# Performance work log

Measured on AMD Instinct MI355X. Metric: run time of the kernel, lower is better.

## Reference

```python
import jax, jax.numpy as jnp
import numpy as np


def _segment_mean(x, idx, num_segments):
    # mean-aggregate rows of x into num_segments buckets (PyG SAGEConv default aggr)
    s = jax.ops.segment_sum(x, idx, num_segments=num_segments)
    c = jax.ops.segment_sum(jnp.ones((idx.shape[0],), x.dtype), idx, num_segments=num_segments)
    return s / jnp.maximum(c, 1.0)[:, None]


def setup_inputs() -> dict:
    key = jax.random.key(0)
    ks = jax.random.split(key, 12)
    N_LIG, N_PROT, D, H, E = 100000, 50000, 64, 128, 2000000
    sc = 0.05
    return {
        "x_lig": jax.random.normal(ks[0], (N_LIG, D), jnp.float32),
        "x_prot": jax.random.normal(ks[1], (N_PROT, D), jnp.float32),
        "W_l_lp": jax.random.normal(ks[2], (D, H), jnp.float32) * sc,
        "b_lp": jnp.zeros((H,), jnp.float32),
        "W_r_lp": jax.random.normal(ks[3], (D, H), jnp.float32) * sc,
        "W_l_pl": jax.random.normal(ks[4], (D, H), jnp.float32) * sc,
        "b_pl": jnp.zeros((H,), jnp.float32),
        "W_r_pl": jax.random.normal(ks[5], (D, H), jnp.float32) * sc,
        "W_lin": jax.random.normal(ks[6], (H, 1), jnp.float32) * sc,
        "b_lin": jnp.zeros((1,), jnp.float32),
        "src_lp": jax.random.randint(ks[7], (E,), 0, N_LIG, jnp.int32),
        "dst_lp": jax.random.randint(ks[8], (E,), 0, N_PROT, jnp.int32),
        "src_pl": jax.random.randint(ks[9], (E,), 0, N_PROT, jnp.int32),
        "dst_pl": jax.random.randint(ks[10], (E,), 0, N_LIG, jnp.int32),
    }


def reference(x_lig, x_prot, W_l_lp, b_lp, W_r_lp, W_l_pl, b_pl, W_r_pl,
              W_lin, b_lin, src_lp, dst_lp, src_pl, dst_pl):
    n_lig = x_lig.shape[0]
    n_prot = x_prot.shape[0]
    # SAGEConv ('ligand','interacts','protein'): gather ligand feats along edges, mean into proteins
    agg_prot = _segment_mean(x_lig[src_lp], dst_lp, n_prot)          # [N_prot, D]
    h_prot = jax.nn.relu(agg_prot @ W_l_lp + b_lp + x_prot @ W_r_lp)  # [N_prot, H] (dead downstream, as in original)
    # SAGEConv ('protein','interacts','ligand')
    agg_lig = _segment_mean(x_prot[src_pl], dst_pl, n_lig)           # [N_lig, D]
    h_lig = jax.nn.relu(agg_lig @ W_l_pl + b_pl + x_lig @ W_r_pl)    # [N_lig, H]
    ligand_out = h_lig.mean(axis=0)                                  # [H]
    del h_prot  # original computes it but never uses it (only 'ligand' feeds the head)
    return ligand_out @ W_lin + b_lin                                # [1]
```

## Files before the change

kernel.cpp:

```cpp
#include <hip/hip_runtime.h>

#define D 64
#define H 128
#define BN 128
#define CAP 3456
#define NBB 256
#define CE 7816

typedef short bf16x8 __attribute__((ext_vector_type(8)));
typedef float f32x4  __attribute__((ext_vector_type(4)));

__device__ __forceinline__ ushort f2bf(float f) {
    unsigned u = __float_as_uint(f);
    unsigned r = (u + 0x7FFFu + ((u >> 16) & 1u)) >> 16;
    return (ushort)r;
}

__device__ __forceinline__ bf16x8 pack8(float4 a, float4 b) {
    ushort o[8];
    o[0]=f2bf(a.x); o[1]=f2bf(a.y); o[2]=f2bf(a.z); o[3]=f2bf(a.w);
    o[4]=f2bf(b.x); o[5]=f2bf(b.y); o[6]=f2bf(b.z); o[7]=f2bf(b.w);
    bf16x8 r;
    __builtin_memcpy(&r, o, 16);
    return r;
}

__global__ __launch_bounds__(256)
void stage1_kernel(const float* __restrict__ xp, ushort* __restrict__ xpb, int totalp,
                   const float* __restrict__ Wl, const float* __restrict__ Wr,
                   ushort* __restrict__ wprep,
                   const int* __restrict__ dst, int* __restrict__ cnt,
                   int E, int K, int ce, int PB) {
    __shared__ int scnt[800];
    int bid = blockIdx.x;
    int t = threadIdx.x;
    if (bid < PB) {
        int i = (bid * 256 + t) * 8;
        if (i < totalp) {
            float4 a = *(const float4*)(xp + i);
            float4 b = *(const float4*)(xp + i + 4);
            bf16x8 v = pack8(a, b);
            *(bf16x8*)(xpb + i) = v;
        }
    } else if (bid < PB + 8) {
        int e = (bid - PB) * 256 + t;
        if (e < 2048) {
            int lane = e & 63;
            int ks = (e >> 6) & 3;
            int ht = e >> 8;
            int h = ht * 16 + (lane & 15);
            int k0 = ks * 32 + (lane >> 4) * 8;
            ushort o[8];
            #pragma unroll
            for (int j = 0; j < 8; ++j) {
                int k = k0 + j;
                float v = (k < D) ? Wl[k * H + h] : Wr[(k - D) * H + h];
                o[j] = f2bf(v);
            }
            *(bf16x8*)(wprep + (size_t)e * 8) = *(bf16x8*)o;
        }
    } else {
        int blk = bid - PB - 8;
        for (int b = t; b < 800; b += 256) scnt[b] = 0;
        __syncthreads();
        int e0 = blk * ce;
        int e1 = min(E, e0 + ce);
        for (int i = e0 + t * 4; i < e1; i += 1024) {
            int4 d4 = *(const int4*)(dst + i);
            atomicAdd(&scnt[d4.x >> 7], 1);
            atomicAdd(&scnt[d4.y >> 7], 1);
            atomicAdd(&scnt[d4.z >> 7], 1);
            atomicAdd(&scnt[d4.w >> 7], 1);
        }
        __syncthreads();
        int* row = cnt + (size_t)blk * K;
        for (int b = t; b < K; b += 256) row[b] = scnt[b];
    }
}

__global__ __launch_bounds__(NBB)
void part_scan_kernel(const int* __restrict__ cnt, int* __restrict__ off,
                      int* __restrict__ tot, int K) {
    __shared__ int s[NBB];
    int b = blockIdx.x;
    int t = threadIdx.x;
    int v = cnt[(size_t)t * K + b];
    s[t] = v;
    __syncthreads();
    for (int o = 1; o < NBB; o <<= 1) {
        int x = (t >= o) ? s[t - o] : 0;
        __syncthreads();
        s[t] += x;
        __syncthreads();
    }
    off[(size_t)t * K + b] = s[t] - v;
    if (t == NBB - 1) tot[b] = s[t];
}

__global__ __launch_bounds__(512)
void part_scatter_kernel(const int* __restrict__ src, const int* __restrict__ dst,
                         const int* __restrict__ off, int* __restrict__ gb,
                         int E, int K, int ce) {
    __shared__ int shist[800];
    __shared__ int sbase[800];
    __shared__ int gdelta[800];
    __shared__ int lcur[800];
    __shared__ int sscan[512];
    __shared__ int ebuf[CE];
    __shared__ unsigned short bkt[CE];

    int blk = blockIdx.x, t = threadIdx.x;
    int e0 = blk * ce;
    int e1 = min(E, e0 + ce);
    int myn = e1 - e0;

    for (int b = t; b < 800; b += 512) shist[b] = 0;
    __syncthreads();
    for (int i = e0 + t * 4; i < e1; i += 2048) {
        int4 d4 = *(const int4*)(dst + i);
        atomicAdd(&shist[d4.x >> 7], 1);
        atomicAdd(&shist[d4.y >> 7], 1);
        atomicAdd(&shist[d4.z >> 7], 1);
        atomicAdd(&shist[d4.w >> 7], 1);
    }
    __syncthreads();
    int c0 = 0, c1 = 0;
    if (t < 400) { c0 = shist[2 * t]; c1 = shist[2 * t + 1]; }
    int cs = c0 + c1;
    sscan[t] = (t < 400) ? cs : 0;
    __syncthreads();
    for (int o = 1; o < 512; o <<= 1) {
        int x = (t >= o) ? sscan[t - o] : 0;
        __syncthreads();
        sscan[t] += x;
        __syncthreads();
    }
    if (t < 400) {
        int ex = sscan[t] - cs;
        sbase[2 * t] = ex;
        sbase[2 * t + 1] = ex + c0;
    }
    __syncthreads();
    const int* orow = off + (size_t)blk * K;
    for (int b = t; b < K; b += 512) {
        int sb = sbase[b];
        gdelta[b] = orow[b] - sb;
        lcur[b] = sb;
    }
    __syncthreads();
    for (int i = e0 + t * 4; i < e1; i += 2048) {
        int4 d4 = *(const int4*)(dst + i);
        int4 s4 = *(const int4*)(src + i);
        int b, p;
        b = d4.x >> 7; p = atomicAdd(&lcur[b], 1);
        ebuf[p] = (s4.x & 0xFFFF) | ((d4.x & 127) << 16); bkt[p] = (unsigned short)b;
        b = d4.y >> 7; p = atomicAdd(&lcur[b], 1);
        ebuf[p] = (s4.y & 0xFFFF) | ((d4.y & 127) << 16); bkt[p] = (unsigned short)b;
        b = d4.z >> 7; p = atomicAdd(&lcur[b], 1);
        ebuf[p] = (s4.z & 0xFFFF) | ((d4.z & 127) << 16); bkt[p] = (unsigned short)b;
        b = d4.w >> 7; p = atomicAdd(&lcur[b], 1);
        ebuf[p] = (s4.w & 0xFFFF) | ((d4.w & 127) << 16); bkt[p] = (unsigned short)b;
    }
    __syncthreads();
    for (int p = t; p < myn; p += 512) {
        int b = bkt[p];
        int loc = gdelta[b] + p;
        if (loc < CAP) gb[(size_t)b * CAP + loc] = ebuf[p];
    }
}

__global__ __launch_bounds__(512, 4)
void fused_kernel(const ushort* __restrict__ xpb, const float* __restrict__ x_lig,
                  const int* __restrict__ gtot, const int* __restrict__ gb,
                  const ushort* __restrict__ wprep, const float* __restrict__ bvec,
                  float* __restrict__ pgrid, int N) {
    __shared__ int sdeg[BN];
    __shared__ int sstart[BN];
    __shared__ int scur[BN];
    __shared__ int ssc[BN];
    __shared__ int scsr[CAP];
    __shared__ unsigned sxrow[8][16][34];
    __shared__ float sred[8][H];

    int b = blockIdx.x, t = threadIdx.x;
    int cnt = min(gtot[b], CAP);
    const int* mygb = gb + (size_t)b * CAP;

    if (t < BN) sdeg[t] = 0;
    __syncthreads();
    for (int i = t; i < cnt; i += 512)
        atomicAdd(&sdeg[mygb[i] >> 16], 1);
    __syncthreads();
    if (t < BN) ssc[t] = sdeg[t];
    __syncthreads();
    for (int off = 1; off < BN; off <<= 1) {
        int v = 0;
        if (t < BN && t >= off) v = ssc[t - off];
        __syncthreads();
        if (t < BN) ssc[t] += v;
        __syncthreads();
    }
    if (t < BN) {
        int ex = ssc[t] - sdeg[t];
        sstart[t] = ex;
        scur[t] = ex;
    }
    __syncthreads();
    for (int i = t; i < cnt; i += 512) {
        int e = mygb[i];
        int p = atomicAdd(&scur[e >> 16], 1);
        scsr[p] = e & 0xFFFF;
    }
    __syncthreads();

    int wv = t >> 6, lane = t & 63;
    int sub = lane >> 3, part = lane & 7;

    for (int i = 0; i < 16; ++i) {
        int ln = wv * 16 + i;
        int s0 = sstart[ln], dg = sdeg[ln];
        float a[8] = {0.f,0.f,0.f,0.f,0.f,0.f,0.f,0.f};
        int j = sub;
        for (; j + 8 < dg; j += 16) {
            uint4 v0 = *(const uint4*)(xpb + (size_t)scsr[s0 + j] * D + part * 8);
            uint4 v1 = *(const uint4*)(xpb + (size_t)scsr[s0 + j + 8] * D + part * 8);
            a[0] += __uint_as_float(v0.x << 16); a[1] += __uint_as_float(v0.x & 0xFFFF0000u);
            a[2] += __uint_as_float(v0.y << 16); a[3] += __uint_as_float(v0.y & 0xFFFF0000u);
            a[4] += __uint_as_float(v0.z << 16); a[5] += __uint_as_float(v0.z & 0xFFFF0000u);
            a[6] += __uint_as_float(v0.w << 16); a[7] += __uint_as_float(v0.w & 0xFFFF0000u);
            a[0] += __uint_as_float(v1.x << 16); a[1] += __uint_as_float(v1.x & 0xFFFF0000u);
            a[2] += __uint_as_float(v1.y << 16); a[3] += __uint_as_float(v1.y & 0xFFFF0000u);
            a[4] += __uint_as_float(v1.z << 16); a[5] += __uint_as_float(v1.z & 0xFFFF0000u);
            a[6] += __uint_as_float(v1.w << 16); a[7] += __uint_as_float(v1.w & 0xFFFF0000u);
        }
        if (j < dg) {
            uint4 v0 = *(const uint4*)(xpb + (size_t)scsr[s0 + j] * D + part * 8);
            a[0] += __uint_as_float(v0.x << 16); a[1] += __uint_as_float(v0.x & 0xFFFF0000u);
            a[2] += __uint_as_float(v0.y << 16); a[3] += __uint_as_float(v0.y & 0xFFFF0000u);
            a[4] += __uint_as_float(v0.z << 16); a[5] += __uint_as_float(v0.z & 0xFFFF0000u);
            a[6] += __uint_as_float(v0.w << 16); a[7] += __uint_as_float(v0.w & 0xFFFF0000u);
        }
        #pragma unroll
        for (int k = 0; k < 8; ++k) {
            a[k] += __shfl_xor(a[k], 8);
            a[k] += __shfl_xor(a[k], 16);
            a[k] += __shfl_xor(a[k], 32);
        }
        if (sub == 0) {
            float inv = 1.0f / fmaxf((float)dg, 1.0f);
            unsigned p0 = (unsigned)f2bf(a[0]*inv) | ((unsigned)f2bf(a[1]*inv) << 16);
            unsigned p1 = (unsigned)f2bf(a[2]*inv) | ((unsigned)f2bf(a[3]*inv) << 16);
            unsigned p2 = (unsigned)f2bf(a[4]*inv) | ((unsigned)f2bf(a[5]*inv) << 16);
            unsigned p3 = (unsigned)f2bf(a[6]*inv) | ((unsigned)f2bf(a[7]*inv) << 16);
            uint2* w2 = (uint2*)&sxrow[wv][i][part * 4];
            w2[0] = make_uint2(p0, p1);
            w2[1] = make_uint2(p2, p3);
        }
    }

    int r = lane & 15, kg = lane >> 4;

    unsigned ua0[4], ua1[4];
    const unsigned* rp = &sxrow[wv][r][0];
    #pragma unroll
    for (int j2 = 0; j2 < 4; ++j2) {
        ua0[j2] = rp[kg * 4 + j2];
        ua1[j2] = rp[16 + kg * 4 + j2];
    }
    bf16x8 A0, A1;
    __builtin_memcpy(&A0, ua0, 16);
    __builtin_memcpy(&A1, ua1, 16);

    int grow = b * BN + wv * 16 + r;
    bf16x8 A2, A3;
    if (grow < N) {
        const float* xr = x_lig + (size_t)grow * D;
        float4 va = *(const float4*)(xr + kg * 8);
        float4 vb = *(const float4*)(xr + kg * 8 + 4);
        A2 = pack8(va, vb);
        float4 vc = *(const float4*)(xr + 32 + kg * 8);
        float4 vd = *(const float4*)(xr + 32 + kg * 8 + 4);
        A3 = pack8(vc, vd);
    } else {
        A2 = bf16x8{0,0,0,0,0,0,0,0};
        A3 = A2;
    }

    float hsum[8];
    bool full = (b * BN + wv * 16 + 16 <= N);
    const bf16x8* wp = (const bf16x8*)wprep;
    #pragma unroll 2
    for (int ht = 0; ht < 8; ++ht) {
        f32x4 acc = {0.f, 0.f, 0.f, 0.f};
        acc = __builtin_amdgcn_mfma_f32_16x16x32_bf16(A0, wp[(ht*4+0)*64 + lane], acc, 0, 0, 0);
        acc = __builtin_amdgcn_mfma_f32_16x16x32_bf16(A1, wp[(ht*4+1)*64 + lane], acc, 0, 0, 0);
        acc = __builtin_amdgcn_mfma_f32_16x16x32_bf16(A2, wp[(ht*4+2)*64 + lane], acc, 0, 0, 0);
        acc = __builtin_amdgcn_mfma_f32_16x16x32_bf16(A3, wp[(ht*4+3)*64 + lane], acc, 0, 0, 0);
        float bb = bvec[ht * 16 + r];
        float s = 0.f;
        if (full) {
            #pragma unroll
            for (int i = 0; i < 4; ++i) s += fmaxf(acc[i] + bb, 0.f);
        } else {
            #pragma unroll
            for (int i = 0; i < 4; ++i) {
                int row = b * BN + wv * 16 + kg * 4 + i;
                if (row < N) s += fmaxf(acc[i] + bb, 0.f);
            }
        }
        hsum[ht] = s;
    }

    #pragma unroll
    for (int ht = 0; ht < 8; ++ht) {
        float v = hsum[ht];
        v += __shfl_xor(v, 16);
        v += __shfl_xor(v, 32);
        if (lane < 16) sred[wv][ht * 16 + lane] = v;
    }
    __syncthreads();
    if (t < H) {
        float s = 0.f;
        #pragma unroll
        for (int w = 0; w < 8; ++w) s += sred[w][t];
        pgrid[(size_t)b * H + t] = s;
    }
}

__global__ __launch_bounds__(128)
void reduce1_kernel(const float* __restrict__ pgrid, int nb, float* __restrict__ pgrid2) {
    int t = threadIdx.x;
    float s = 0.f;
    for (int r = blockIdx.x; r < nb; r += 64) s += pgrid[(size_t)r * H + t];
    pgrid2[(size_t)blockIdx.x * H + t] = s;
}

__global__ __launch_bounds__(128)
void head_kernel(const float* __restrict__ pgrid2,
                 const float* __restrict__ W_lin, const float* __restrict__ b_lin,
                 float* __restrict__ out, float invN) {
    __shared__ float sh[H];
    int t = threadIdx.x;
    float s = 0.f;
    #pragma unroll 8
    for (int r = 0; r < 64; ++r) s += pgrid2[(size_t)r * H + t];
    sh[t] = s * invN * W_lin[t];
    __syncthreads();
    if (t == 0) {
        float tot = b_lin[0];
        for (int i = 0; i < H; ++i) tot += sh[i];
        out[0] = tot;
    }
}

extern "C" void kernel_launch(void* const* d_in, const int* in_sizes, int n_in,
                              void* d_out, int out_size, void* d_ws, size_t ws_size,
                              hipStream_t stream) {
    const float* x_lig  = (const float*)d_in[0];
    const float* x_prot = (const float*)d_in[1];
    const float* W_l_pl = (const float*)d_in[5];
    const float* b_pl   = (const float*)d_in[6];
    const float* W_r_pl = (const float*)d_in[7];
    const float* W_lin  = (const float*)d_in[8];
    const float* b_lin  = (const float*)d_in[9];
    const int*   src_pl = (const int*)d_in[12];
    const int*   dst_pl = (const int*)d_in[13];

    int N  = in_sizes[0] / D;
    int NP = in_sizes[1] / D;
    int E  = in_sizes[12];
    int K  = (N + BN - 1) / BN;

    char* base = (char*)d_ws;
    ushort* xpb   = (ushort*)base;  base += (size_t)NP * D * sizeof(ushort);
    float* pgrid  = (float*)base;   base += (size_t)K * H * sizeof(float);
    float* pgrid2 = (float*)base;   base += (size_t)64 * H * sizeof(float);
    ushort* wprep = (ushort*)base;  base += (size_t)2048 * 8 * sizeof(ushort);
    int* cnt      = (int*)base;     base += (size_t)NBB * K * sizeof(int);
    int* off      = (int*)base;     base += (size_t)NBB * K * sizeof(int);
    int* tot      = (int*)base;     base += (size_t)K * sizeof(int);
    base = (char*)(((size_t)base + 255) & ~(size_t)255);
    int* gb       = (int*)base;     base += (size_t)K * CAP * sizeof(int);

    int ce = ((E + NBB - 1) / NBB + 3) & ~3;
    int PB = (NP * D / 8 + 255) / 256;

    stage1_kernel<<<PB + 8 + NBB, 256, 0, stream>>>(x_prot, xpb, NP * D,
                                                    W_l_pl, W_r_pl, wprep,
                                                    dst_pl, cnt, E, K, ce, PB);
    part_scan_kernel<<<K, NBB, 0, stream>>>(cnt, off, tot, K);
    part_scatter_kernel<<<NBB, 512, 0, stream>>>(src_pl, dst_pl, off, gb, E, K, ce);
    fused_kernel<<<K, 512, 0, stream>>>(xpb, x_lig, tot, gb, wprep, b_pl, pgrid, N);
    reduce1_kernel<<<64, 128, 0, stream>>>(pgrid, K, pgrid2);
    head_kernel<<<1, 128, 0, stream>>>(pgrid2, W_lin, b_lin, (float*)d_out,
                                       1.0f / (float)N);
}
```

Before: 96.11 us.

## Gather neighbor features directly into MFMA operand layout per lane

Replaces the per-node cooperative gather (8 sub-groups of lanes per node plus shuffle reductions and an LDS staging buffer) with a scheme where each lane gathers and accumulates the features its own MFMA A-fragment needs. This removes the cross-lane shuffle reduction, the shared-memory row buffer and its readback. In exchange each lane walks a whole neighbor list serially, so lanes with different degrees diverge and each wave has fewer independent loads in flight per node.

Result: no change. 95.94 us (-0.2%).

```diff
diff --git a/kernel.cpp b/kernel.cpp
--- a/kernel.cpp
+++ b/kernel.cpp
@@ -23,6 +23,13 @@
     bf16x8 r;
     __builtin_memcpy(&r, o, 16);
     return r;
+}
+
+__device__ __forceinline__ void accu(float* a, uint4 v) {
+    a[0] += __uint_as_float(v.x << 16); a[1] += __uint_as_float(v.x & 0xFFFF0000u);
+    a[2] += __uint_as_float(v.y << 16); a[3] += __uint_as_float(v.y & 0xFFFF0000u);
+    a[4] += __uint_as_float(v.z << 16); a[5] += __uint_as_float(v.z & 0xFFFF0000u);
+    a[6] += __uint_as_float(v.w << 16); a[7] += __uint_as_float(v.w & 0xFFFF0000u);
 }
 
 __global__ __launch_bounds__(256)
@@ -179,7 +186,6 @@
     __shared__ int scur[BN];
     __shared__ int ssc[BN];
     __shared__ int scsr[CAP];
-    __shared__ unsigned sxrow[8][16][34];
     __shared__ float sred[8][H];
 
     int b = blockIdx.x, t = threadIdx.x;
@@ -214,62 +220,43 @@
     __syncthreads();
 
     int wv = t >> 6, lane = t & 63;
-    int sub = lane >> 3, part = lane & 7;
-
-    for (int i = 0; i < 16; ++i) {
-        int ln = wv * 16 + i;
-        int s0 = sstart[ln], dg = sdeg[ln];
-        float a[8] = {0.f,0.f,0.f,0.f,0.f,0.f,0.f,0.f};
-        int j = sub;
-        for (; j + 8 < dg; j += 16) {
-            uint4 v0 = *(const uint4*)(xpb + (size_t)scsr[s0 + j] * D + part * 8);
-            uint4 v1 = *(const uint4*)(xpb + (size_t)scsr[s0 + j + 8] * D + part * 8);
-            a[0] += __uint_as_float(v0.x << 16); a[1] += __uint_as_float(v0.x & 0xFFFF0000u);
-            a[2] += __uint_as_float(v0.y << 16); a[3] += __uint_as_float(v0.y & 0xFFFF0000u);
-            a[4] += __uint_as_float(v0.z << 16); a[5] += __uint_as_float(v0.z & 0xFFFF0000u);
-            a[6] += __uint_as_float(v0.w << 16); a[7] += __uint_as_float(v0.w & 0xFFFF0000u);
-            a[0] += __uint_as_float(v1.x << 16); a[1] += __uint_as_float(v1.x & 0xFFFF0000u);
-            a[2] += __uint_as_float(v1.y << 16); a[3] += __uint_as_float(v1.y & 0xFFFF0000u);
-            a[4] += __uint_as_float(v1.z << 16); a[5] += __uint_as_float(v1.z & 0xFFFF0000u);
-            a[6] += __uint_as_float(v1.w << 16); a[7] += __uint_as_float(v1.w & 0xFFFF0000u);
-        }
-        if (j < dg) {
-            uint4 v0 = *(const uint4*)(xpb + (size_t)scsr[s0 + j] * D + part * 8);
-            a[0] += __uint_as_float(v0.x << 16); a[1] += __uint_as_float(v0.x & 0xFFFF0000u);
-            a[2] += __uint_as_float(v0.y << 16); a[3] += __uint_as_float(v0.y & 0xFFFF0000u);
-            a[4] += __uint_as_float(v0.z << 16); a[5] += __uint_as_float(v0.z & 0xFFFF0000u);
-            a[6] += __uint_as_float(v0.w << 16); a[7] += __uint_as_float(v0.w & 0xFFFF0000u);
-        }
-        #pragma unroll
-        for (int k = 0; k < 8; ++k) {
-            a[k] += __shfl_xor(a[k], 8);
-            a[k] += __shfl_xor(a[k], 16);
-            a[k] += __shfl_xor(a[k], 32);
-        }
-        if (sub == 0) {
-            float inv = 1.0f / fmaxf((float)dg, 1.0f);
-            unsigned p0 = (unsigned)f2bf(a[0]*inv) | ((unsigned)f2bf(a[1]*inv) << 16);
-            unsigned p1 = (unsigned)f2bf(a[2]*inv) | ((unsigned)f2bf(a[3]*inv) << 16);
-            unsigned p2 = (unsigned)f2bf(a[4]*inv) | ((unsigned)f2bf(a[5]*inv) << 16);
-            unsigned p3 = (unsigned)f2bf(a[6]*inv) | ((unsigned)f2bf(a[7]*inv) << 16);
-            uint2* w2 = (uint2*)&sxrow[wv][i][part * 4];
-            w2[0] = make_uint2(p0, p1);
-            w2[1] = make_uint2(p2, p3);
-        }
-    }
-
     int r = lane & 15, kg = lane >> 4;
 
-    unsigned ua0[4], ua1[4];
-    const unsigned* rp = &sxrow[wv][r][0];
+    int ln = wv * 16 + r;
+    int s0 = sstart[ln], dg = sdeg[ln];
+    float a0[8] = {0.f,0.f,0.f,0.f,0.f,0.f,0.f,0.f};
+    float a1[8] = {0.f,0.f,0.f,0.f,0.f,0.f,0.f,0.f};
+    int j = 0;
+    for (; j + 1 < dg; j += 2) {
+        int i0 = scsr[s0 + j];
+        int i1 = scsr[s0 + j + 1];
+        const ushort* r0 = xpb + (size_t)i0 * D + kg * 8;
+        const ushort* r1 = xpb + (size_t)i1 * D + kg * 8;
+        uint4 u0 = *(const uint4*)(r0);
+        uint4 u1 = *(const uint4*)(r0 + 32);
+        uint4 w0 = *(const uint4*)(r1);
+        uint4 w1 = *(const uint4*)(r1 + 32);
+        accu(a0, u0); accu(a1, u1);
+        accu(a0, w0); accu(a1, w1);
+    }
+    if (j < dg) {
+        int i0 = scsr[s0 + j];
+        const ushort* r0 = xpb + (size_t)i0 * D + kg * 8;
+        uint4 u0 = *(const uint4*)(r0);
+        uint4 u1 = *(const uint4*)(r0 + 32);
+        accu(a0, u0); accu(a1, u1);
+    }
+
+    float inv = 1.0f / fmaxf((float)dg, 1.0f);
+    ushort o0[8], o1[8];
     #pragma unroll
-    for (int j2 = 0; j2 < 4; ++j2) {
-        ua0[j2] = rp[kg * 4 + j2];
-        ua1[j2] = rp[16 + kg * 4 + j2];
+    for (int k = 0; k < 8; ++k) {
+        o0[k] = f2bf(a0[k] * inv);
+        o1[k] = f2bf(a1[k] * inv);
     }
     bf16x8 A0, A1;
-    __builtin_memcpy(&A0, ua0, 16);
-    __builtin_memcpy(&A1, ua1, 16);
+    __builtin_memcpy(&A0, o0, 16);
+    __builtin_memcpy(&A1, o1, 16);
 
     int grow = b * BN + wv * 16 + r;
     bf16x8 A2, A3;
```
